# Performance work log

Measured on AMD Instinct MI355X. Metric: run time of the kernel, lower is better.

## Reference

```python
import jax, jax.numpy as jnp
import numpy as np

# Dimensions: batch B, window W (time features), nodes M, hidden HID, hops NLAYERS
B, W, M, HID, NLAYERS = 32, 168, 2048, 128, 6


def setup_inputs() -> dict:
    key = jax.random.key(0)
    ks = jax.random.split(key, 6)
    x = jax.random.normal(ks[0], (B, W, M), dtype=jnp.float32)
    # scale L so matrix powers L^k stay bounded (spectral radius < 1)
    L = jax.random.normal(ks[1], (M, M), dtype=jnp.float32) / (2.0 * np.float32(np.sqrt(M)))
    # stacked per-hop MLP params: linears[i]: W->HID, linears2[i]: HID->1
    W1 = jax.random.normal(ks[2], (NLAYERS + 1, HID, W), dtype=jnp.float32) / np.float32(np.sqrt(W))
    b1 = jax.random.normal(ks[3], (NLAYERS + 1, HID), dtype=jnp.float32) * 0.01
    W2 = jax.random.normal(ks[4], (NLAYERS + 1, HID), dtype=jnp.float32) / np.float32(np.sqrt(HID))
    b2 = jax.random.normal(ks[5], (NLAYERS + 1,), dtype=jnp.float32) * 0.01
    return {"x": x, "L": L, "W1": W1, "b1": b1, "W2": W2, "b2": b2}


def _hop_mlp(t, w1, bb1, w2, bb2):
    # t: [B, M, W] -> scalar score per node: Linear(W->HID), ReLU, Linear(HID->1)
    h = jax.nn.relu(jnp.einsum('bmw,hw->bmh', t, w1) + bb1)
    return jnp.einsum('bmh,h->bm', h, w2) + bb2


def reference(x, L, W1, b1, W2, b2):
    xt = jnp.swapaxes(x, 1, 2)  # [B, M, W] (x.transpose(2,1))
    s = _hop_mlp(xt, W1[0], b1[0], W2[0], b2[0])  # [B, M]
    P = L
    for i in range(1, NLAYERS + 1):
        # PP.expand + bmm == broadcasted matmul; never materialize [B,M,M]
        t = jnp.einsum('ij,bjw->biw', P, xt)  # [B, M, W]
        s = s + _hop_mlp(t, W1[i], b1[i], W2[i], b2[i])
        P = jnp.matmul(L, P)  # next graph power
    return s  # [B, M]; output_fun is None so no final nonlinearity
```

## Files before the change

### kernel.cpp

```cpp
#include <hip/hip_runtime.h>
#include <cstdint>
#include <cstddef>

typedef __bf16 bf16_t;
typedef __attribute__((ext_vector_type(8))) __bf16 bf16x8;
typedef __attribute__((ext_vector_type(4))) __bf16 bf16x4;
typedef __attribute__((ext_vector_type(4))) float floatx4;

#define NB 32
#define NW 168
#define NM 2048
#define NHID 128
#define NBW (NB * NW)
#define NGEMM 168
#define NMLPB 512

#define GLOAD_LDS16(g, l)                                          \
  __builtin_amdgcn_global_load_lds(                                \
      (const __attribute__((address_space(1))) void*)(g),          \
      (__attribute__((address_space(3))) void*)(l), 16, 0, 0)

__global__ void cast_bf16_kernel(const float* __restrict__ in, bf16_t* __restrict__ out, int n4) {
  int stride = gridDim.x * blockDim.x;
  for (int i = blockIdx.x * blockDim.x + threadIdx.x; i < n4; i += stride) {
    float4 v = ((const float4*)in)[i];
    bf16x4 o = {(bf16_t)v.x, (bf16_t)v.y, (bf16_t)v.z, (bf16_t)v.w};
    ((bf16x4*)out)[i] = o;
  }
}

__global__ void prep_x_kernel(const float* __restrict__ x, bf16_t* __restrict__ Xb,
                              bf16_t* __restrict__ XT) {
  __shared__ float tile[64][65];
  const int R = NBW, C = NM;
  int r0 = blockIdx.y * 64, c0 = blockIdx.x * 64;
  int t = threadIdx.x;
  int tr = t >> 4, tc4 = (t & 15) * 4;
#pragma unroll
  for (int p = 0; p < 4; ++p) {
    int row = p * 16 + tr;
    float4 v = *(const float4*)(x + (size_t)(r0 + row) * C + c0 + tc4);
    tile[row][tc4 + 0] = v.x;
    tile[row][tc4 + 1] = v.y;
    tile[row][tc4 + 2] = v.z;
    tile[row][tc4 + 3] = v.w;
    bf16x4 o = {(bf16_t)v.x, (bf16_t)v.y, (bf16_t)v.z, (bf16_t)v.w};
    *(bf16x4*)(Xb + (size_t)(r0 + row) * C + c0 + tc4) = o;
  }
  __syncthreads();
#pragma unroll
  for (int p = 0; p < 4; ++p) {
    int c = p * 16 + tr;
    bf16x4 o = {(bf16_t)tile[tc4 + 0][c], (bf16_t)tile[tc4 + 1][c],
                (bf16_t)tile[tc4 + 2][c], (bf16_t)tile[tc4 + 3][c]};
    *(bf16x4*)(XT + (size_t)(c0 + c) * R + r0 + tc4) = o;
  }
}

__device__ __forceinline__ void mlp_single(
    int tid, int r0, bf16_t* __restrict__ Bs,
    const bf16_t* __restrict__ T, const bf16_t* __restrict__ Wh,
    const float* __restrict__ b1h, const float* __restrict__ w2h, float b2v,
    float* __restrict__ out, int accumulate) {
  float* sred = (float*)(Bs + 24576);
  int lane = tid & 63, wv2 = tid >> 6;

#pragma unroll
  for (int i = 0; i < 6; ++i) {
    int c = i * 512 + tid;
    if (c >= 2688) {
      int4 z = {0, 0, 0, 0};
      *(int4*)(Bs + (size_t)c * 8) = z;
    } else {
      int kc = c >> 7;
      int h = (c & 127) ^ ((kc & 3) << 2);
      GLOAD_LDS16(Wh + (size_t)h * NW + kc * 8, Bs + (size_t)(i * 512 + wv2 * 64) * 8);
    }
  }
  __syncthreads();

  if (tid < 256) {
    int wm = wv2 >> 1, wn = wv2 & 1;
    int quad = lane >> 4, l15 = lane & 15;
    const bf16_t* arow[4];
#pragma unroll
    for (int mi = 0; mi < 4; ++mi) {
      int R = r0 + wm * 64 + mi * 16 + l15;
      arow[mi] = T + (size_t)(R >> 5) * NBW + (size_t)(R & 31) * NW + quad * 8;
    }
    floatx4 zero4 = {0.f, 0.f, 0.f, 0.f};
    floatx4 acc[4][4];
#pragma unroll
    for (int mi = 0; mi < 4; ++mi)
#pragma unroll
      for (int ni = 0; ni < 4; ++ni) acc[mi][ni] = zero4;

#pragma unroll
    for (int kb = 0; kb < 192; kb += 32) {
      int kc = (kb >> 3) + quad;
      bf16x8 af[4], bf[4];
#pragma unroll
      for (int mi = 0; mi < 4; ++mi)
        af[mi] = *(const bf16x8*)(arow[mi] + kb);
#pragma unroll
      for (int ni = 0; ni < 4; ++ni) {
        int hpos = (wn * 64 + ni * 16 + l15) ^ ((kc & 3) << 2);
        bf[ni] = *(const bf16x8*)(Bs + (size_t)(kc * 128 + hpos) * 8);
      }
#pragma unroll
      for (int mi = 0; mi < 4; ++mi)
#pragma unroll
        for (int ni = 0; ni < 4; ++ni)
          acc[mi][ni] = __builtin_amdgcn_mfma_f32_16x16x32_bf16(af[mi], bf[ni], acc[mi][ni], 0, 0, 0);
    }

    float part[4][4];
#pragma unroll
    for (int mi = 0; mi < 4; ++mi)
#pragma unroll
      for (int r = 0; r < 4; ++r) part[mi][r] = 0.f;
#pragma unroll
    for (int ni = 0; ni < 4; ++ni) {
      int col = wn * 64 + ni * 16 + l15;
      float b1v = b1h[col];
      float w2v = w2h[col];
#pragma unroll
      for (int mi = 0; mi < 4; ++mi)
#pragma unroll
        for (int r = 0; r < 4; ++r) {
          float h = acc[mi][ni][r] + b1v;
          h = h > 0.f ? h : 0.f;
          part[mi][r] += h * w2v;
        }
    }
#pragma unroll
    for (int off = 1; off < 16; off <<= 1)
#pragma unroll
      for (int mi = 0; mi < 4; ++mi)
#pragma unroll
        for (int r = 0; r < 4; ++r) part[mi][r] += __shfl_xor(part[mi][r], off);
    if (l15 == 0) {
#pragma unroll
      for (int mi = 0; mi < 4; ++mi)
#pragma unroll
        for (int r = 0; r < 4; ++r) sred[wv2 * 64 + mi * 16 + quad * 4 + r] = part[mi][r];
    }
  }
  __syncthreads();
  if (tid < 128) {
    int hh = tid >> 6;
    int lr = tid & 63;
    float v = sred[(hh * 2) * 64 + lr] + sred[(hh * 2 + 1) * 64 + lr] + b2v;
    int R = r0 + hh * 64 + lr;
    int idx = (R & 31) * NM + (R >> 5);
    if (accumulate)
      out[idx] += v;
    else
      out[idx] = v;
  }
}

#define STAGE2(gbase, ld, t, ks, ldsbase)                                        \
  do {                                                                           \
    const bf16_t* _g = (gbase) + (size_t)(t) * 64 + (ks) * 32;                   \
    GLOAD_LDS16(_g, lds + (ldsbase) + (ks) * 8192 + wv * 512);                   \
    GLOAD_LDS16(_g + (size_t)128 * (ld),                                         \
                lds + (ldsbase) + (ks) * 8192 + 4096 + wv * 512);                \
  } while (0)

#define VM6 asm volatile("s_waitcnt vmcnt(6)" ::: "memory")
#define TOPB asm volatile("s_barrier" ::: "memory")
#define ENDB __builtin_amdgcn_s_barrier()

#define RD_A(dst, bufoff, ks, mh)                                                \
  _Pragma("unroll") for (int mi = 0; mi < 4; ++mi)                               \
      dst[mi] = *(const bf16x8*)(pA + (bufoff) + (ks) * 8192 + ((mh) * 4 + mi) * 512)

#define RD_B(dst, bufoff, ks)                                                    \
  _Pragma("unroll") for (int ni = 0; ni < 4; ++ni)                               \
      dst[ni] = *(const bf16x8*)(pB + (bufoff) + (ks) * 8192 + ni * 512)

#define MM16(af_, bf_, mh)                                                       \
  do {                                                                           \
    __builtin_amdgcn_s_setprio(1);                                               \
    _Pragma("unroll") for (int mi = 0; mi < 4; ++mi)                             \
        _Pragma("unroll") for (int ni = 0; ni < 4; ++ni)                         \
            acc[(mh) * 4 + mi][ni] = __builtin_amdgcn_mfma_f32_16x16x32_bf16(    \
                af_[mi], bf_[ni], acc[(mh) * 4 + mi][ni], 0, 0, 0);              \
    __builtin_amdgcn_s_setprio(0);                                               \
  } while (0)

__global__ __launch_bounds__(512, 2) void fused_gemm_mlp_kernel(
    const bf16_t* __restrict__ A, const bf16_t* __restrict__ Bt,
    bf16_t* __restrict__ C, bf16_t* __restrict__ Ct,
    int K, int lda, int ldb, int ldc, int ldct, int write_c,
    const bf16_t* __restrict__ T, const bf16_t* __restrict__ W1b,
    const float* __restrict__ b1, const float* __restrict__ W2,
    const float* __restrict__ b2, float* __restrict__ out,
    int hop, int accumulate) {
  __shared__ bf16_t lds[65536];
  const int bx = blockIdx.x;
  const int tid = threadIdx.x;

  if (bx >= NGEMM) {
    int j = bx - NGEMM;
    mlp_single(tid, j * 128, lds, T, W1b + (size_t)hop * NHID * NW,
               b1 + hop * NHID, W2 + hop * NHID, b2[hop], out, accumulate);
    return;
  }

  const int m0 = (bx >> 3) * 256, n0 = (bx & 7) * 256;
  const int lane = tid & 63, wv = tid >> 6;
  const int wm = wv >> 2, wn = wv & 3;
  const int quad = lane >> 4, l15 = lane & 15;

  const int srow = tid >> 2;
  const int scsw = (tid & 3) ^ ((srow >> 1) & 3);
  const bf16_t* aS = A + (size_t)(m0 + srow) * lda + scsw * 8;
  const bf16_t* bS = Bt + (size_t)(n0 + srow) * ldb + scsw * 8;

  const int fsw = (quad ^ ((l15 >> 1) & 3)) * 8;
  const bf16_t* pA = lds + (size_t)(wm * 128 + l15) * 32 + fsw;
  const bf16_t* pB = lds + 16384 + (size_t)(wn * 64 + l15) * 32 + fsw;

  floatx4 zero4 = {0.f, 0.f, 0.f, 0.f};
  floatx4 acc[8][4];
#pragma unroll
  for (int mi = 0; mi < 8; ++mi)
#pragma unroll
    for (int ni = 0; ni < 4; ++ni) acc[mi][ni] = zero4;

  STAGE2(aS, lda, 0, 0, 0);
  STAGE2(bS, ldb, 0, 0, 16384);
  STAGE2(aS, lda, 0, 1, 0);
  STAGE2(bS, ldb, 0, 1, 16384);
  STAGE2(aS, lda, 1, 0, 32768);
  STAGE2(bS, ldb, 1, 0, 49152);
  asm volatile("s_waitcnt vmcnt(8)" ::: "memory");
  TOPB;

  bf16x8 af0[4], af1[4], bf0[4], bf1[4];
  RD_B(bf0, 0, 0);
  RD_A(af0, 0, 0, 0);

  const int nt = K >> 6;
  const int nit = K >> 7;
#pragma unroll 1
  for (int i = 0; i < nit; ++i) {
    const int t1 = 2 * i + 1;
    const int t2 = (t1 + 1 < nt) ? t1 + 1 : 0;
    const int t3 = (t1 + 2 < nt) ? t1 + 2 : 0;
    RD_A(af1, 0, 0, 1);
    MM16(af0, bf0, 0);
    STAGE2(aS, lda, t1, 1, 32768);
    ENDB;
    VM6; TOPB;
    RD_B(bf1, 0, 1);
    RD_A(af0, 0, 1, 0);
    MM16(af1, bf0, 1);
    STAGE2(bS, ldb, t1, 1, 49152);
    ENDB;
    RD_A(af1, 0, 1, 1);
    MM16(af0, bf1, 0);
    STAGE2(aS, lda, t2, 0, 0);
    ENDB;
    VM6; TOPB;
    RD_B(bf0, 32768, 0);
    RD_A(af0, 32768, 0, 0);
    MM16(af1, bf1, 1);
    STAGE2(bS, ldb, t2, 0, 16384);
    ENDB;
    RD_A(af1, 32768, 0, 1);
    MM16(af0, bf0, 0);
    STAGE2(aS, lda, t2, 1, 0);
    ENDB;
    VM6; TOPB;
    RD_B(bf1, 32768, 1);
    RD_A(af0, 32768, 1, 0);
    MM16(af1, bf0, 1);
    STAGE2(bS, ldb, t2, 1, 16384);
    ENDB;
    RD_A(af1, 32768, 1, 1);
    MM16(af0, bf1, 0);
    STAGE2(aS, lda, t3, 0, 32768);
    ENDB;
    VM6; TOPB;
    RD_B(bf0, 0, 0);
    RD_A(af0, 0, 0, 0);
    MM16(af1, bf1, 1);
    STAGE2(bS, ldb, t3, 0, 49152);
    ENDB;
  }
  asm volatile("s_waitcnt vmcnt(0)" ::: "memory");

#pragma unroll
  for (int mi = 0; mi < 8; ++mi) {
#pragma unroll
    for (int ni = 0; ni < 4; ++ni) {
      int col = n0 + wn * 64 + ni * 16 + l15;
      int rowb = m0 + wm * 128 + mi * 16 + quad * 4;
      bf16x4 tv;
#pragma unroll
      for (int r = 0; r < 4; ++r) tv[r] = (bf16_t)acc[mi][ni][r];
      *(bf16x4*)(Ct + (size_t)col * ldct + rowb) = tv;
      if (write_c) {
#pragma unroll
        for (int r = 0; r < 4; ++r)
          C[(size_t)(rowb + r) * ldc + col] = tv[r];
      }
    }
  }
}

__global__ __launch_bounds__(512) void mlp_score_kernel(
    const bf16_t* __restrict__ T, const bf16_t* __restrict__ W1b,
    const float* __restrict__ b1, const float* __restrict__ W2,
    const float* __restrict__ b2, float* __restrict__ out,
    int hop, int accumulate) {
  __shared__ bf16_t Bs[24 * 128 * 8 + 512];
  mlp_single(threadIdx.x, blockIdx.x * 128, Bs, T,
             W1b + (size_t)hop * NHID * NW, b1 + hop * NHID, W2 + hop * NHID,
             b2[hop], out, accumulate);
}

extern "C" void kernel_launch(void* const* d_in, const int* in_sizes, int n_in,
                              void* d_out, int out_size, void* d_ws, size_t ws_size,
                              hipStream_t stream) {
  const float* x = (const float*)d_in[0];
  const float* L = (const float*)d_in[1];
  const float* W1 = (const float*)d_in[2];
  const float* b1 = (const float*)d_in[3];
  const float* W2 = (const float*)d_in[4];
  const float* b2 = (const float*)d_in[5];
  float* out = (float*)d_out;

  char* ws = (char*)d_ws;
  size_t off = 0;
  auto walloc = [&](size_t bytes) -> void* {
    off = (off + 255) & ~(size_t)255;
    void* p = ws + off;
    off += bytes;
    return p;
  };
  bf16_t* Xb = (bf16_t*)walloc((size_t)NBW * NM * 2);
  bf16_t* XT0 = (bf16_t*)walloc((size_t)NM * NBW * 2);
  bf16_t* XT1 = (bf16_t*)walloc((size_t)NM * NBW * 2);
  bf16_t* Lb = (bf16_t*)walloc((size_t)NM * NM * 2);
  bf16_t* W1b = (bf16_t*)walloc((size_t)7 * NHID * NW * 2);
  bf16_t* Ta = (bf16_t*)walloc((size_t)NBW * NM * 2);
  (void)ws_size; (void)in_sizes; (void)n_in; (void)out_size;

  prep_x_kernel<<<dim3(NM / 64, NBW / 64), dim3(256), 0, stream>>>(x, Xb, XT0);
  cast_bf16_kernel<<<dim3(1024), dim3(256), 0, stream>>>(L, Lb, NM * NM / 4);
  cast_bf16_kernel<<<dim3(64), dim3(256), 0, stream>>>(W1, W1b, 7 * NHID * NW / 4);

  bf16_t* src = Xb;
  bf16_t* dst = Ta;
  bf16_t* xtprev = XT0;
  bf16_t* xtcur = XT1;
  for (int i = 1; i <= 6; ++i) {
    fused_gemm_mlp_kernel<<<dim3(NGEMM + NMLPB), dim3(512), 0, stream>>>(
        src, Lb, dst, xtcur, NM, NM, NM, NM, NBW, (i < 6) ? 1 : 0,
        xtprev, W1b, b1, W2, b2, out, i - 1, (i > 1) ? 1 : 0);
    bf16_t* t = src; src = dst; dst = t;
    t = xtprev; xtprev = xtcur; xtcur = t;
  }
  mlp_score_kernel<<<dim3(NM * NB / 128), dim3(512), 0, stream>>>(
      xtprev, W1b, b1, W2, b2, out, 6, 1);
}
```

Measured before the change: 466.0 us.

## Restructure GEMM main loop to single A-fragment buffer with lockstep barriers

Replaces the software-pipelined register double-buffering of A fragments (LDS reads overlapped with the previous MFMA block) with a single fragment buffer. Each phase now reads from LDS, waits for lgkmcnt(0), and then issues MFMAs, with more barriers and a vmcnt(8) wait. The goal is to cut VGPR pressure and simplify the ordering of global-to-LDS staging. The cost is that LDS read latency is no longer hidden behind MFMA work, and the extra barriers add synchronization.

```diff
diff --git a/kernel.cpp b/kernel.cpp
--- a/kernel.cpp
+++ b/kernel.cpp
@@ -168,19 +168,19 @@
                 lds + (ldsbase) + (ks) * 8192 + 4096 + wv * 512);                \
   } while (0)
 
-#define VM6 asm volatile("s_waitcnt vmcnt(6)" ::: "memory")
-#define TOPB asm volatile("s_barrier" ::: "memory")
-#define ENDB __builtin_amdgcn_s_barrier()
-
-#define RD_A(dst, bufoff, ks, mh)                                                \
+#define VM8 asm volatile("s_waitcnt vmcnt(8)" ::: "memory")
+#define BAR __builtin_amdgcn_s_barrier()
+#define LG0 asm volatile("s_waitcnt lgkmcnt(0)" ::: "memory")
+
+#define RD_A4(dst, bufoff, ks, mh)                                               \
   _Pragma("unroll") for (int mi = 0; mi < 4; ++mi)                               \
       dst[mi] = *(const bf16x8*)(pA + (bufoff) + (ks) * 8192 + ((mh) * 4 + mi) * 512)
 
-#define RD_B(dst, bufoff, ks)                                                    \
+#define RD_B4(dst, bufoff, ks)                                                   \
   _Pragma("unroll") for (int ni = 0; ni < 4; ++ni)                               \
       dst[ni] = *(const bf16x8*)(pB + (bufoff) + (ks) * 8192 + ni * 512)
 
-#define MM16(af_, bf_, mh)                                                       \
+#define MM(af_, bf_, mh)                                                         \
   do {                                                                           \
     __builtin_amdgcn_s_setprio(1);                                               \
     _Pragma("unroll") for (int mi = 0; mi < 4; ++mi)                             \
@@ -236,13 +236,10 @@
   STAGE2(bS, ldb, 0, 1, 16384);
   STAGE2(aS, lda, 1, 0, 32768);
   STAGE2(bS, ldb, 1, 0, 49152);
-  asm volatile("s_waitcnt vmcnt(8)" ::: "memory");
-  TOPB;
-
-  bf16x8 af0[4], af1[4], bf0[4], bf1[4];
-  RD_B(bf0, 0, 0);
-  RD_A(af0, 0, 0, 0);
-
+  VM8;
+  BAR;
+
+  bf16x8 af[4], bf0[4], bf1[4];
   const int nt = K >> 6;
   const int nit = K >> 7;
 #pragma unroll 1
@@ -250,46 +247,50 @@
     const int t1 = 2 * i + 1;
     const int t2 = (t1 + 1 < nt) ? t1 + 1 : 0;
     const int t3 = (t1 + 2 < nt) ? t1 + 2 : 0;
-    RD_A(af1, 0, 0, 1);
-    MM16(af0, bf0, 0);
+    RD_B4(bf0, 0, 0);
+    RD_A4(af, 0, 0, 0);
     STAGE2(aS, lda, t1, 1, 32768);
-    ENDB;
-    VM6; TOPB;
-    RD_B(bf1, 0, 1);
-    RD_A(af0, 0, 1, 0);
-    MM16(af1, bf0, 1);
+    BAR; LG0;
+    MM(af, bf0, 0);
+    BAR;
+    RD_A4(af, 0, 0, 1);
     STAGE2(bS, ldb, t1, 1, 49152);
-    ENDB;
-    RD_A(af1, 0, 1, 1);
-    MM16(af0, bf1, 0);
+    BAR; LG0;
+    MM(af, bf0, 1);
+    VM8; BAR;
+    RD_B4(bf1, 0, 1);
+    RD_A4(af, 0, 1, 0);
     STAGE2(aS, lda, t2, 0, 0);
-    ENDB;
-    VM6; TOPB;
-    RD_B(bf0, 32768, 0);
-    RD_A(af0, 32768, 0, 0);
-    MM16(af1, bf1, 1);
+    BAR; LG0;
+    MM(af, bf1, 0);
+    BAR;
+    RD_A4(af, 0, 1, 1);
     STAGE2(bS, ldb, t2, 0, 16384);
-    ENDB;
-    RD_A(af1, 32768, 0, 1);
-    MM16(af0, bf0, 0);
+    BAR; LG0;
+    MM(af, bf1, 1);
+    VM8; BAR;
+    RD_B4(bf0, 32768, 0);
+    RD_A4(af, 32768, 0, 0);
     STAGE2(aS, lda, t2, 1, 0);
-    ENDB;
-    VM6; TOPB;
-    RD_B(bf1, 32768, 1);
-    RD_A(af0, 32768, 1, 0);
-    MM16(af1, bf0, 1);
+    BAR; LG0;
+    MM(af, bf0, 0);
+    BAR;
+    RD_A4(af, 32768, 0, 1);
     STAGE2(bS, ldb, t2, 1, 16384);
-    ENDB;
-    RD_A(af1, 32768, 1, 1);
-    MM16(af0, bf1, 0);
+    BAR; LG0;
+    MM(af, bf0, 1);
+    VM8; BAR;
+    RD_B4(bf1, 32768, 1);
+    RD_A4(af, 32768, 1, 0);
     STAGE2(aS, lda, t3, 0, 32768);
-    ENDB;
-    VM6; TOPB;
-    RD_B(bf0, 0, 0);
-    RD_A(af0, 0, 0, 0);
-    MM16(af1, bf1, 1);
+    BAR; LG0;
+    MM(af, bf1, 0);
+    BAR;
+    RD_A4(af, 32768, 1, 1);
     STAGE2(bS, ldb, t3, 0, 49152);
-    ENDB;
+    BAR; LG0;
+    MM(af, bf1, 1);
+    VM8; BAR;
   }
   asm volatile("s_waitcnt vmcnt(0)" ::: "memory");
 
```

After: 482.9 us. +3.6%, slower.
